# Performance work log

Measured on AMD Instinct MI355X. Metric: run time of the kernel, lower is better.

## Reference

```python
import jax, jax.numpy as jnp
import numpy as np

N_NODES = 1_000_000
N_EDGES = 32_000_000
NUM_HOP = 3


def setup_inputs() -> dict:
    key = jax.random.key(0)
    k1, k2 = jax.random.split(key)
    h = jnp.ones((N_NODES, 1), dtype=jnp.float32)  # graph.ndata['one']
    src = jax.random.randint(k1, (N_EDGES,), 0, N_NODES, dtype=jnp.int64 if jax.config.read('jax_enable_x64') else jnp.int32)
    dst = jax.random.randint(k2, (N_EDGES,), 0, N_NODES, dtype=jnp.int64 if jax.config.read('jax_enable_x64') else jnp.int32)
    # SAGEConv weights, init to ones per reset_parameters(); bias=False
    w_self = jnp.ones((NUM_HOP, 1, 1), dtype=jnp.float32)
    w_neigh = jnp.ones((NUM_HOP, 1, 1), dtype=jnp.float32)
    return {"h": h, "src": src, "dst": dst, "w_self": w_self, "w_neigh": w_neigh}


def reference(h, src, dst, w_self, w_neigh):
    # Stacked SAGEConv(aggregator='add', bias=False, feat_drop=0):
    #   h_out = h @ W_self + segment_sum(h[src] -> dst) @ W_neigh
    # dropout p=0 between layers is identity.
    n = h.shape[0]
    num_hop = w_self.shape[0]
    for i in range(num_hop):
        neigh = jax.ops.segment_sum(h[src], dst, num_segments=n)  # [N, F] sum over in-edges
        h = h @ w_self[i] + neigh @ w_neigh[i]
    return h
```

## Files before the change

kernel.cpp:

```cpp
#include <hip/hip_runtime.h>


typedef unsigned u32x4 __attribute__((ext_vector_type(4)));
typedef float    f32x4 __attribute__((ext_vector_type(4)));

constexpr int BLK      = 256;
constexpr int BBITS    = 13;
constexpr int BUCKET   = 1 << BBITS;
constexpr int SEGSHIFT = 17;
constexpr int NSEG     = 8;
constexpr int SEGB     = 3;
constexpr int KMAX     = 1024;
constexpr int SPLIT    = 4;
constexpr int TILE     = 8192;
constexpr int HBLOCKS  = 1024;
constexpr unsigned SRCMASK = (1u << SEGSHIFT) - 1u;


__global__ void zero_u32(unsigned* __restrict__ p, int n) {
    int i = blockIdx.x * blockDim.x + threadIdx.x;
    if (i < n) p[i] = 0u;
}

__global__ void hist_kernel(const int* __restrict__ dst, const int* __restrict__ src,
                            int ne, unsigned* __restrict__ count, int nk) {
    __shared__ unsigned hist[KMAX * 4];
    for (int b = threadIdx.x; b < KMAX * 4; b += blockDim.x) hist[b] = 0u;
    __syncthreads();
    const u32x4* dst4 = reinterpret_cast<const u32x4*>(dst);
    const u32x4* src4 = reinterpret_cast<const u32x4*>(src);
    int nvec = ne >> 2;
    int sub = threadIdx.x & 3;
    for (int i = blockIdx.x * blockDim.x + threadIdx.x; i < nvec;
         i += gridDim.x * blockDim.x) {
        u32x4 d = __builtin_nontemporal_load(dst4 + i);
        u32x4 s = __builtin_nontemporal_load(src4 + i);
        atomicAdd(&hist[((((d.x >> BBITS) << SEGB) | (s.x >> SEGSHIFT)) << 2) | sub], 1u);
        atomicAdd(&hist[((((d.y >> BBITS) << SEGB) | (s.y >> SEGSHIFT)) << 2) | sub], 1u);
        atomicAdd(&hist[((((d.z >> BBITS) << SEGB) | (s.z >> SEGSHIFT)) << 2) | sub], 1u);
        atomicAdd(&hist[((((d.w >> BBITS) << SEGB) | (s.w >> SEGSHIFT)) << 2) | sub], 1u);
    }
    if (blockIdx.x == 0 && threadIdx.x == 0)
        for (int i = nvec << 2; i < ne; ++i) {
            unsigned key = (((unsigned)dst[i] >> BBITS) << SEGB) |
                           ((unsigned)src[i] >> SEGSHIFT);
            atomicAdd(&hist[key << 2], 1u);
        }
    __syncthreads();
    for (int b = threadIdx.x; b < nk; b += blockDim.x) {
        unsigned v = hist[b * 4] + hist[b * 4 + 1] + hist[b * 4 + 2] + hist[b * 4 + 3];
        if (v) atomicAdd(&count[b], v);
    }
}

__global__ void scan_kernel(const unsigned* __restrict__ count,
                            unsigned* __restrict__ offsets,
                            unsigned* __restrict__ cursor, int nk) {
    __shared__ unsigned s[KMAX];
    int t = threadIdx.x;
    unsigned v  = (t < nk) ? count[t] : 0u;
    unsigned pv = (v + 3u) & ~3u;
    s[t] = pv;
    __syncthreads();
    for (int d = 1; d < KMAX; d <<= 1) {
        unsigned u = (t >= d) ? s[t - d] : 0u;
        __syncthreads();
        s[t] += u;
        __syncthreads();
    }
    unsigned excl = s[t] - pv;
    if (t < nk) { offsets[t] = excl; cursor[t] = excl; }
}

__global__ __launch_bounds__(1024)
void bin_kernel(const int* __restrict__ src, const int* __restrict__ dst, int ne,
                unsigned* __restrict__ cursor, unsigned* __restrict__ recs) {
    __shared__ unsigned hist[KMAX];
    __shared__ unsigned start[KMAX];
    __shared__ unsigned lpos[KMAX];
    __shared__ unsigned rec[TILE];
    __shared__ unsigned short kid[TILE];

    int base = blockIdx.x * TILE;
    int cnt = min(TILE, ne - base);
    if (cnt <= 0) return;

    hist[threadIdx.x] = 0u;
    __syncthreads();

    int nvec = cnt & ~3;
    const u32x4* dst4 = reinterpret_cast<const u32x4*>(dst + base);
    const u32x4* src4 = reinterpret_cast<const u32x4*>(src + base);

    for (int i = threadIdx.x; i < (nvec >> 2); i += blockDim.x) {
        u32x4 d = dst4[i];
        u32x4 s = src4[i];
        atomicAdd(&hist[((d.x >> BBITS) << SEGB) | (s.x >> SEGSHIFT)], 1u);
        atomicAdd(&hist[((d.y >> BBITS) << SEGB) | (s.y >> SEGSHIFT)], 1u);
        atomicAdd(&hist[((d.z >> BBITS) << SEGB) | (s.z >> SEGSHIFT)], 1u);
        atomicAdd(&hist[((d.w >> BBITS) << SEGB) | (s.w >> SEGSHIFT)], 1u);
    }
    if (threadIdx.x == 0)
        for (int i = nvec; i < cnt; ++i) {
            unsigned key = (((unsigned)dst[base + i] >> BBITS) << SEGB) |
                           ((unsigned)src[base + i] >> SEGSHIFT);
            atomicAdd(&hist[key], 1u);
        }
    __syncthreads();

    {
        int t = threadIdx.x;
        unsigned v = hist[t];
        start[t] = v;
        __syncthreads();
        for (int d = 1; d < KMAX; d <<= 1) {
            unsigned u = (t >= d) ? start[t - d] : 0u;
            __syncthreads();
            start[t] += u;
            __syncthreads();
        }
        unsigned excl = start[t] - v;
        __syncthreads();
        start[t] = excl;
        lpos[t]  = excl;
        if (v) hist[t] = atomicAdd(&cursor[t], v);
        __syncthreads();
    }

    for (int i = threadIdx.x; i < (nvec >> 2); i += blockDim.x) {
        u32x4 d = __builtin_nontemporal_load(dst4 + i);
        u32x4 s = __builtin_nontemporal_load(src4 + i);
        unsigned dd[4] = {d.x, d.y, d.z, d.w};
        unsigned ss[4] = {s.x, s.y, s.z, s.w};
#pragma unroll
        for (int k = 0; k < 4; ++k) {
            unsigned key = ((dd[k] >> BBITS) << SEGB) | (ss[k] >> SEGSHIFT);
            unsigned p = atomicAdd(&lpos[key], 1u);
            rec[p] = ((dd[k] & (BUCKET - 1)) << SEGSHIFT) | (ss[k] & SRCMASK);
            kid[p] = (unsigned short)key;
        }
    }
    if (threadIdx.x == 0)
        for (int i = nvec; i < cnt; ++i) {
            unsigned dd = (unsigned)dst[base + i], ss = (unsigned)src[base + i];
            unsigned key = ((dd >> BBITS) << SEGB) | (ss >> SEGSHIFT);
            unsigned p = atomicAdd(&lpos[key], 1u);
            rec[p] = ((dd & (BUCKET - 1)) << SEGSHIFT) | (ss & SRCMASK);
            kid[p] = (unsigned short)key;
        }
    __syncthreads();

    for (int i = threadIdx.x; i < cnt; i += blockDim.x) {
        int k = kid[i];
        recs[hist[k] + ((unsigned)i - start[k])] = rec[i];
    }
}

__global__ __launch_bounds__(1024, 8)
void agg_kernel(const float* __restrict__ curh,
                const unsigned* __restrict__ recs,
                const unsigned* __restrict__ offsets,
                const unsigned* __restrict__ count,
                float* __restrict__ partials) {
    __shared__ float acc[BUCKET];
    int b = blockIdx.x >> 2;
    int s = blockIdx.x & 3;
    for (int i = threadIdx.x; i < BUCKET; i += 1024) acc[i] = 0.0f;
    __syncthreads();
#pragma unroll 1
    for (int seg = 0; seg < NSEG; ++seg) {
        unsigned k   = ((unsigned)b << SEGB) | (unsigned)seg;
        unsigned bs  = offsets[k];
        unsigned cnt = count[k];
        unsigned qlen = (cnt >> 2) & ~3u;
        unsigned ss = bs + (unsigned)s * qlen;
        unsigned sc = (s == SPLIT - 1) ? (cnt - 3u * qlen) : qlen;
        const float* ch = curh + ((unsigned)seg << SEGSHIFT);
        unsigned n4 = sc >> 2;
        const u32x4* rq = reinterpret_cast<const u32x4*>(recs + ss);
        for (unsigned q = threadIdx.x; q < n4; q += 1024) {
            u32x4 r = __builtin_nontemporal_load(rq + q);
            float v0 = ch[r.x & SRCMASK];
            float v1 = ch[r.y & SRCMASK];
            float v2 = ch[r.z & SRCMASK];
            float v3 = ch[r.w & SRCMASK];
            atomicAdd(&acc[r.x >> SEGSHIFT], v0);
            atomicAdd(&acc[r.y >> SEGSHIFT], v1);
            atomicAdd(&acc[r.z >> SEGSHIFT], v2);
            atomicAdd(&acc[r.w >> SEGSHIFT], v3);
        }
        if (s == SPLIT - 1) {
            unsigned tb = ss + (n4 << 2);
            unsigned rem = sc & 3u;
            if (threadIdx.x < rem) {
                unsigned r = recs[tb + threadIdx.x];
                atomicAdd(&acc[r >> SEGSHIFT], ch[r & SRCMASK]);
            }
        }
    }
    __syncthreads();
    float* outp = partials + ((size_t)blockIdx.x) * BUCKET;
    for (int i = threadIdx.x; i < BUCKET; i += 1024)
        __builtin_nontemporal_store(acc[i], outp + i);
}

__global__ void reduce_combine(const float* __restrict__ curh,
                               const float* __restrict__ partials,
                               const float* __restrict__ w_self,
                               const float* __restrict__ w_neigh, int hop,
                               float* __restrict__ out, int n) {
    int i = blockIdx.x * blockDim.x + threadIdx.x;
    int nq = (n + 3) >> 2;
    if (i >= nq) return;
    int node = i << 2;
    float wsv = w_self[hop], wnv = w_neigh[hop];
    int b = node >> BBITS, l = node & (BUCKET - 1);
    const float* p0 = partials + ((size_t)b * SPLIT) * BUCKET + l;
    if (node + 3 < n) {
        f32x4 a0 = __builtin_nontemporal_load(reinterpret_cast<const f32x4*>(p0));
        f32x4 a1 = __builtin_nontemporal_load(reinterpret_cast<const f32x4*>(p0 + BUCKET));
        f32x4 a2 = __builtin_nontemporal_load(reinterpret_cast<const f32x4*>(p0 + 2 * BUCKET));
        f32x4 a3 = __builtin_nontemporal_load(reinterpret_cast<const f32x4*>(p0 + 3 * BUCKET));
        f32x4 hh = *reinterpret_cast<const f32x4*>(curh + node);
        f32x4 o = hh * wsv + ((a0 + a1) + (a2 + a3)) * wnv;
        *reinterpret_cast<f32x4*>(out + node) = o;
    } else {
        for (int j = node; j < n; ++j) {
            int bb = j >> BBITS, ll = j & (BUCKET - 1);
            const float* pp = partials + ((size_t)bb * SPLIT) * BUCKET + ll;
            out[j] = curh[j] * wsv +
                     (pp[0] + pp[BUCKET] + pp[2 * BUCKET] + pp[3 * BUCKET]) * wnv;
        }
    }
}


__global__ void zero_f32(float* __restrict__ p, int n) {
    int i = blockIdx.x * blockDim.x + threadIdx.x;
    if (i < n) p[i] = 0.0f;
}

__global__ void scatter_add(const float* __restrict__ h, const int* __restrict__ src,
                            const int* __restrict__ dst, float* __restrict__ neigh, int ne) {
    int i = blockIdx.x * blockDim.x + threadIdx.x;
    int base = i * 4;
    if (base + 3 < ne) {
        int4 s = *reinterpret_cast<const int4*>(src + base);
        int4 d = *reinterpret_cast<const int4*>(dst + base);
        atomicAdd(&neigh[d.x], h[s.x]);
        atomicAdd(&neigh[d.y], h[s.y]);
        atomicAdd(&neigh[d.z], h[s.z]);
        atomicAdd(&neigh[d.w], h[s.w]);
    } else if (base < ne) {
        for (int e = base; e < ne; ++e) atomicAdd(&neigh[dst[e]], h[src[e]]);
    }
}

__global__ void combine(const float* __restrict__ h, const float* __restrict__ neigh,
                        const float* __restrict__ w_self, const float* __restrict__ w_neigh,
                        int hop, float* __restrict__ out, int n) {
    int i = blockIdx.x * blockDim.x + threadIdx.x;
    if (i < n) out[i] = h[i] * w_self[hop] + neigh[i] * w_neigh[hop];
}


extern "C" void kernel_launch(void* const* d_in, const int* in_sizes, int n_in,
                              void* d_out, int out_size, void* d_ws, size_t ws_size,
                              hipStream_t stream) {
    const float* h       = (const float*)d_in[0];
    const int*   src     = (const int*)d_in[1];
    const int*   dst     = (const int*)d_in[2];
    const float* w_self  = (const float*)d_in[3];
    const float* w_neigh = (const float*)d_in[4];
    float* out = (float*)d_out;

    const int n    = in_sizes[0];
    const int ne   = in_sizes[1];
    const int hops = in_sizes[3];

    const int nb = (n + BUCKET - 1) >> BBITS;
    const int nk = nb * NSEG;

    size_t off = 0;
    auto take = [&](size_t bytes) { size_t o = off; off = (off + bytes + 255) & ~255UL; return o; };
    size_t o_recs     = take(((size_t)ne + 4 * KMAX) * 4);
    size_t o_count    = take((size_t)KMAX * 4);
    size_t o_offsets  = take((size_t)KMAX * 4);
    size_t o_cursor   = take((size_t)KMAX * 4);
    size_t o_partials = take((size_t)nb * SPLIT * BUCKET * 4);
    size_t o_buf      = take((size_t)n * 4);
    size_t needed = off;

    char* ws = (char*)d_ws;
    bool fast = (ws_size >= needed) && (nk <= KMAX) && (n <= (1 << 20));

    if (fast) {
        unsigned* recs     = (unsigned*)(ws + o_recs);
        unsigned* count    = (unsigned*)(ws + o_count);
        unsigned* offsets  = (unsigned*)(ws + o_offsets);
        unsigned* cursor   = (unsigned*)(ws + o_cursor);
        float*    partials = (float*)(ws + o_partials);
        float*    buf      = (float*)(ws + o_buf);

        zero_u32<<<(KMAX + BLK - 1) / BLK, BLK, 0, stream>>>(count, KMAX);
        hist_kernel<<<HBLOCKS, BLK, 0, stream>>>(dst, src, ne, count, nk);
        scan_kernel<<<1, KMAX, 0, stream>>>(count, offsets, cursor, nk);
        bin_kernel<<<(ne + TILE - 1) / TILE, KMAX, 0, stream>>>(src, dst, ne, cursor, recs);

        const int nq = (n + 3) >> 2;
        const int gridQ = (nq + BLK - 1) / BLK;
        const float* cur = h;
        for (int hop = 0; hop < hops; ++hop) {
            float* nxt = (hop == hops - 1) ? out : buf;
            agg_kernel<<<nb * SPLIT, 1024, 0, stream>>>(cur, recs, offsets, count, partials);
            reduce_combine<<<gridQ, BLK, 0, stream>>>(cur, partials, w_self, w_neigh, hop, nxt, n);
            cur = nxt;
        }
    } else {
        float* buf   = (float*)d_ws;
        float* neigh = buf + n;
        const int gridN = (n + BLK - 1) / BLK;
        const int gridE = ((ne + 3) / 4 + BLK - 1) / BLK;
        const float* cur = h;
        for (int hop = 0; hop < hops; ++hop) {
            float* nxt = (hop == hops - 1) ? out : buf;
            zero_f32<<<gridN, BLK, 0, stream>>>(neigh, n);
            scatter_add<<<gridE, BLK, 0, stream>>>(cur, src, dst, neigh, ne);
            combine<<<gridN, BLK, 0, stream>>>(cur, neigh, w_self, w_neigh, hop, nxt, n);
            cur = nxt;
        }
    }
}
```

Before: 941.3 us.

## Bin edges by destination bucket only and software-pipeline the aggregation gathers

Drops the source-segment dimension from the binning key, so records are grouped only by 4096-node destination buckets. The source index is packed into 20 bits alongside the local destination. The histogram pass no longer reads src, the binning kernel moves to 256-thread blocks, and aggregation uses a 2-way split with a double-buffered loop that issues the next gathers before applying the LDS atomics. This cuts index traffic and per-segment loop overhead. In exchange, gathers into h now span the whole 4MB array instead of a 512KB source segment, which risks worse cache locality.

```diff
diff --git a/kernel.cpp b/kernel.cpp
--- a/kernel.cpp
+++ b/kernel.cpp
@@ -4,17 +4,13 @@
 typedef unsigned u32x4 __attribute__((ext_vector_type(4)));
 typedef float    f32x4 __attribute__((ext_vector_type(4)));
 
-constexpr int BLK      = 256;
-constexpr int BBITS    = 13;
-constexpr int BUCKET   = 1 << BBITS;
-constexpr int SEGSHIFT = 17;
-constexpr int NSEG     = 8;
-constexpr int SEGB     = 3;
-constexpr int KMAX     = 1024;
-constexpr int SPLIT    = 4;
-constexpr int TILE     = 8192;
-constexpr int HBLOCKS  = 1024;
-constexpr unsigned SRCMASK = (1u << SEGSHIFT) - 1u;
+constexpr int BLK     = 256;
+constexpr int BBITS   = 12;
+constexpr int BUCKET  = 1 << BBITS;
+constexpr int NB_MAX  = 256;
+constexpr int SPLIT   = 2;
+constexpr int TILE    = 8192;
+constexpr int HBLOCKS = 1024;
 
 
 __global__ void zero_u32(unsigned* __restrict__ p, int n) {
@@ -22,32 +18,27 @@
     if (i < n) p[i] = 0u;
 }
 
-__global__ void hist_kernel(const int* __restrict__ dst, const int* __restrict__ src,
-                            int ne, unsigned* __restrict__ count, int nk) {
-    __shared__ unsigned hist[KMAX * 4];
-    for (int b = threadIdx.x; b < KMAX * 4; b += blockDim.x) hist[b] = 0u;
+__global__ void hist_kernel(const int* __restrict__ dst, int ne,
+                            unsigned* __restrict__ count, int nb) {
+    __shared__ unsigned hist[NB_MAX * 4];
+    for (int b = threadIdx.x; b < NB_MAX * 4; b += blockDim.x) hist[b] = 0u;
     __syncthreads();
     const u32x4* dst4 = reinterpret_cast<const u32x4*>(dst);
-    const u32x4* src4 = reinterpret_cast<const u32x4*>(src);
     int nvec = ne >> 2;
     int sub = threadIdx.x & 3;
     for (int i = blockIdx.x * blockDim.x + threadIdx.x; i < nvec;
          i += gridDim.x * blockDim.x) {
         u32x4 d = __builtin_nontemporal_load(dst4 + i);
-        u32x4 s = __builtin_nontemporal_load(src4 + i);
-        atomicAdd(&hist[((((d.x >> BBITS) << SEGB) | (s.x >> SEGSHIFT)) << 2) | sub], 1u);
-        atomicAdd(&hist[((((d.y >> BBITS) << SEGB) | (s.y >> SEGSHIFT)) << 2) | sub], 1u);
-        atomicAdd(&hist[((((d.z >> BBITS) << SEGB) | (s.z >> SEGSHIFT)) << 2) | sub], 1u);
-        atomicAdd(&hist[((((d.w >> BBITS) << SEGB) | (s.w >> SEGSHIFT)) << 2) | sub], 1u);
+        atomicAdd(&hist[((d.x >> BBITS) << 2) | sub], 1u);
+        atomicAdd(&hist[((d.y >> BBITS) << 2) | sub], 1u);
+        atomicAdd(&hist[((d.z >> BBITS) << 2) | sub], 1u);
+        atomicAdd(&hist[((d.w >> BBITS) << 2) | sub], 1u);
     }
     if (blockIdx.x == 0 && threadIdx.x == 0)
-        for (int i = nvec << 2; i < ne; ++i) {
-            unsigned key = (((unsigned)dst[i] >> BBITS) << SEGB) |
-                           ((unsigned)src[i] >> SEGSHIFT);
-            atomicAdd(&hist[key << 2], 1u);
-        }
-    __syncthreads();
-    for (int b = threadIdx.x; b < nk; b += blockDim.x) {
+        for (int i = nvec << 2; i < ne; ++i)
+            atomicAdd(&hist[(((unsigned)dst[i] >> BBITS) << 2)], 1u);
+    __syncthreads();
+    for (int b = threadIdx.x; b < nb; b += blockDim.x) {
         unsigned v = hist[b * 4] + hist[b * 4 + 1] + hist[b * 4 + 2] + hist[b * 4 + 3];
         if (v) atomicAdd(&count[b], v);
     }
@@ -55,37 +46,38 @@
 
 __global__ void scan_kernel(const unsigned* __restrict__ count,
                             unsigned* __restrict__ offsets,
-                            unsigned* __restrict__ cursor, int nk) {
-    __shared__ unsigned s[KMAX];
+                            unsigned* __restrict__ cursor, int nb) {
+    __shared__ unsigned s[NB_MAX];
     int t = threadIdx.x;
-    unsigned v  = (t < nk) ? count[t] : 0u;
+    unsigned v  = (t < nb) ? count[t] : 0u;
     unsigned pv = (v + 3u) & ~3u;
     s[t] = pv;
     __syncthreads();
-    for (int d = 1; d < KMAX; d <<= 1) {
+    for (int d = 1; d < NB_MAX; d <<= 1) {
         unsigned u = (t >= d) ? s[t - d] : 0u;
         __syncthreads();
         s[t] += u;
         __syncthreads();
     }
     unsigned excl = s[t] - pv;
-    if (t < nk) { offsets[t] = excl; cursor[t] = excl; }
-}
-
-__global__ __launch_bounds__(1024)
+    if (t < nb) { offsets[t] = excl; cursor[t] = excl; }
+}
+
+__global__ __launch_bounds__(256)
 void bin_kernel(const int* __restrict__ src, const int* __restrict__ dst, int ne,
                 unsigned* __restrict__ cursor, unsigned* __restrict__ recs) {
-    __shared__ unsigned hist[KMAX];
-    __shared__ unsigned start[KMAX];
-    __shared__ unsigned lpos[KMAX];
+    __shared__ unsigned hist[NB_MAX];
+    __shared__ unsigned start[NB_MAX];
+    __shared__ unsigned lpos[NB_MAX];
+    __shared__ unsigned gbase[NB_MAX];
     __shared__ unsigned rec[TILE];
-    __shared__ unsigned short kid[TILE];
+    __shared__ unsigned char bid[TILE];
 
     int base = blockIdx.x * TILE;
     int cnt = min(TILE, ne - base);
     if (cnt <= 0) return;
 
-    hist[threadIdx.x] = 0u;
+    for (int b = threadIdx.x; b < NB_MAX; b += blockDim.x) hist[b] = 0u;
     __syncthreads();
 
     int nvec = cnt & ~3;
@@ -94,18 +86,14 @@
 
     for (int i = threadIdx.x; i < (nvec >> 2); i += blockDim.x) {
         u32x4 d = dst4[i];
-        u32x4 s = src4[i];
-        atomicAdd(&hist[((d.x >> BBITS) << SEGB) | (s.x >> SEGSHIFT)], 1u);
-        atomicAdd(&hist[((d.y >> BBITS) << SEGB) | (s.y >> SEGSHIFT)], 1u);
-        atomicAdd(&hist[((d.z >> BBITS) << SEGB) | (s.z >> SEGSHIFT)], 1u);
-        atomicAdd(&hist[((d.w >> BBITS) << SEGB) | (s.w >> SEGSHIFT)], 1u);
+        atomicAdd(&hist[d.x >> BBITS], 1u);
+        atomicAdd(&hist[d.y >> BBITS], 1u);
+        atomicAdd(&hist[d.z >> BBITS], 1u);
+        atomicAdd(&hist[d.w >> BBITS], 1u);
     }
     if (threadIdx.x == 0)
-        for (int i = nvec; i < cnt; ++i) {
-            unsigned key = (((unsigned)dst[base + i] >> BBITS) << SEGB) |
-                           ((unsigned)src[base + i] >> SEGSHIFT);
-            atomicAdd(&hist[key], 1u);
-        }
+        for (int i = nvec; i < cnt; ++i)
+            atomicAdd(&hist[(unsigned)dst[base + i] >> BBITS], 1u);
     __syncthreads();
 
     {
@@ -113,7 +101,7 @@
         unsigned v = hist[t];
         start[t] = v;
         __syncthreads();
-        for (int d = 1; d < KMAX; d <<= 1) {
+        for (int d = 1; d < NB_MAX; d <<= 1) {
             unsigned u = (t >= d) ? start[t - d] : 0u;
             __syncthreads();
             start[t] += u;
@@ -123,7 +111,7 @@
         __syncthreads();
         start[t] = excl;
         lpos[t]  = excl;
-        if (v) hist[t] = atomicAdd(&cursor[t], v);
+        if (v) gbase[t] = atomicAdd(&cursor[t], v);
         __syncthreads();
     }
 
@@ -134,25 +122,25 @@
         unsigned ss[4] = {s.x, s.y, s.z, s.w};
 #pragma unroll
         for (int k = 0; k < 4; ++k) {
-            unsigned key = ((dd[k] >> BBITS) << SEGB) | (ss[k] >> SEGSHIFT);
-            unsigned p = atomicAdd(&lpos[key], 1u);
-            rec[p] = ((dd[k] & (BUCKET - 1)) << SEGSHIFT) | (ss[k] & SRCMASK);
-            kid[p] = (unsigned short)key;
+            unsigned b = dd[k] >> BBITS;
+            unsigned p = atomicAdd(&lpos[b], 1u);
+            rec[p] = ((dd[k] & (BUCKET - 1)) << 20) | ss[k];
+            bid[p] = (unsigned char)b;
         }
     }
     if (threadIdx.x == 0)
         for (int i = nvec; i < cnt; ++i) {
             unsigned dd = (unsigned)dst[base + i], ss = (unsigned)src[base + i];
-            unsigned key = ((dd >> BBITS) << SEGB) | (ss >> SEGSHIFT);
-            unsigned p = atomicAdd(&lpos[key], 1u);
-            rec[p] = ((dd & (BUCKET - 1)) << SEGSHIFT) | (ss & SRCMASK);
-            kid[p] = (unsigned short)key;
+            unsigned b = dd >> BBITS;
+            unsigned p = atomicAdd(&lpos[b], 1u);
+            rec[p] = ((dd & (BUCKET - 1)) << 20) | ss;
+            bid[p] = (unsigned char)b;
         }
     __syncthreads();
 
     for (int i = threadIdx.x; i < cnt; i += blockDim.x) {
-        int k = kid[i];
-        recs[hist[k] + ((unsigned)i - start[k])] = rec[i];
+        int b = bid[i];
+        recs[gbase[b] + ((unsigned)i - start[b])] = rec[i];
     }
 }
 
@@ -163,40 +151,77 @@
                 const unsigned* __restrict__ count,
                 float* __restrict__ partials) {
     __shared__ float acc[BUCKET];
-    int b = blockIdx.x >> 2;
-    int s = blockIdx.x & 3;
+    int b = blockIdx.x >> 1;
+    int s = blockIdx.x & 1;
     for (int i = threadIdx.x; i < BUCKET; i += 1024) acc[i] = 0.0f;
     __syncthreads();
-#pragma unroll 1
-    for (int seg = 0; seg < NSEG; ++seg) {
-        unsigned k   = ((unsigned)b << SEGB) | (unsigned)seg;
-        unsigned bs  = offsets[k];
-        unsigned cnt = count[k];
-        unsigned qlen = (cnt >> 2) & ~3u;
-        unsigned ss = bs + (unsigned)s * qlen;
-        unsigned sc = (s == SPLIT - 1) ? (cnt - 3u * qlen) : qlen;
-        const float* ch = curh + ((unsigned)seg << SEGSHIFT);
-        unsigned n4 = sc >> 2;
-        const u32x4* rq = reinterpret_cast<const u32x4*>(recs + ss);
-        for (unsigned q = threadIdx.x; q < n4; q += 1024) {
-            u32x4 r = __builtin_nontemporal_load(rq + q);
-            float v0 = ch[r.x & SRCMASK];
-            float v1 = ch[r.y & SRCMASK];
-            float v2 = ch[r.z & SRCMASK];
-            float v3 = ch[r.w & SRCMASK];
-            atomicAdd(&acc[r.x >> SEGSHIFT], v0);
-            atomicAdd(&acc[r.y >> SEGSHIFT], v1);
-            atomicAdd(&acc[r.z >> SEGSHIFT], v2);
-            atomicAdd(&acc[r.w >> SEGSHIFT], v3);
-        }
-        if (s == SPLIT - 1) {
-            unsigned tb = ss + (n4 << 2);
-            unsigned rem = sc & 3u;
-            if (threadIdx.x < rem) {
-                unsigned r = recs[tb + threadIdx.x];
-                atomicAdd(&acc[r >> SEGSHIFT], ch[r & SRCMASK]);
-            }
-        }
+    unsigned bs  = offsets[b];
+    unsigned cnt = count[b];
+    unsigned half = (cnt >> 1) & ~3u;
+    unsigned ss = bs + (s ? half : 0u);
+    unsigned sc = s ? (cnt - half) : half;
+    unsigned n4 = sc >> 2;
+    const u32x4* rq = reinterpret_cast<const u32x4*>(recs + ss);
+
+    unsigned q = threadIdx.x;
+    if (q + 1024 < n4) {
+        u32x4 rA = __builtin_nontemporal_load(rq + q);
+        u32x4 rB = __builtin_nontemporal_load(rq + q + 1024);
+        float a0 = curh[rA.x & 0xFFFFFu];
+        float a1 = curh[rA.y & 0xFFFFFu];
+        float a2 = curh[rA.z & 0xFFFFFu];
+        float a3 = curh[rA.w & 0xFFFFFu];
+        float b0 = curh[rB.x & 0xFFFFFu];
+        float b1 = curh[rB.y & 0xFFFFFu];
+        float b2 = curh[rB.z & 0xFFFFFu];
+        float b3 = curh[rB.w & 0xFFFFFu];
+        q += 2048;
+        for (; q + 1024 < n4; q += 2048) {
+            u32x4 rA2 = __builtin_nontemporal_load(rq + q);
+            u32x4 rB2 = __builtin_nontemporal_load(rq + q + 1024);
+            atomicAdd(&acc[rA.x >> 20], a0);
+            atomicAdd(&acc[rA.y >> 20], a1);
+            atomicAdd(&acc[rA.z >> 20], a2);
+            atomicAdd(&acc[rA.w >> 20], a3);
+            atomicAdd(&acc[rB.x >> 20], b0);
+            atomicAdd(&acc[rB.y >> 20], b1);
+            atomicAdd(&acc[rB.z >> 20], b2);
+            atomicAdd(&acc[rB.w >> 20], b3);
+            rA = rA2; rB = rB2;
+            a0 = curh[rA.x & 0xFFFFFu];
+            a1 = curh[rA.y & 0xFFFFFu];
+            a2 = curh[rA.z & 0xFFFFFu];
+            a3 = curh[rA.w & 0xFFFFFu];
+            b0 = curh[rB.x & 0xFFFFFu];
+            b1 = curh[rB.y & 0xFFFFFu];
+            b2 = curh[rB.z & 0xFFFFFu];
+            b3 = curh[rB.w & 0xFFFFFu];
+        }
+        atomicAdd(&acc[rA.x >> 20], a0);
+        atomicAdd(&acc[rA.y >> 20], a1);
+        atomicAdd(&acc[rA.z >> 20], a2);
+        atomicAdd(&acc[rA.w >> 20], a3);
+        atomicAdd(&acc[rB.x >> 20], b0);
+        atomicAdd(&acc[rB.y >> 20], b1);
+        atomicAdd(&acc[rB.z >> 20], b2);
+        atomicAdd(&acc[rB.w >> 20], b3);
+    }
+    if (q < n4) {
+        u32x4 r = __builtin_nontemporal_load(rq + q);
+        float v0 = curh[r.x & 0xFFFFFu];
+        float v1 = curh[r.y & 0xFFFFFu];
+        float v2 = curh[r.z & 0xFFFFFu];
+        float v3 = curh[r.w & 0xFFFFFu];
+        atomicAdd(&acc[r.x >> 20], v0);
+        atomicAdd(&acc[r.y >> 20], v1);
+        atomicAdd(&acc[r.z >> 20], v2);
+        atomicAdd(&acc[r.w >> 20], v3);
+    }
+    unsigned tb = ss + (n4 << 2);
+    unsigned rem = sc & 3u;
+    if (threadIdx.x < rem) {
+        unsigned r = recs[tb + threadIdx.x];
+        atomicAdd(&acc[r >> 20], curh[r & 0xFFFFFu]);
     }
     __syncthreads();
     float* outp = partials + ((size_t)blockIdx.x) * BUCKET;
@@ -216,20 +241,18 @@
     float wsv = w_self[hop], wnv = w_neigh[hop];
     int b = node >> BBITS, l = node & (BUCKET - 1);
     const float* p0 = partials + ((size_t)b * SPLIT) * BUCKET + l;
+    const float* p1 = p0 + BUCKET;
     if (node + 3 < n) {
-        f32x4 a0 = __builtin_nontemporal_load(reinterpret_cast<const f32x4*>(p0));
-        f32x4 a1 = __builtin_nontemporal_load(reinterpret_cast<const f32x4*>(p0 + BUCKET));
-        f32x4 a2 = __builtin_nontemporal_load(reinterpret_cast<const f32x4*>(p0 + 2 * BUCKET));
-        f32x4 a3 = __builtin_nontemporal_load(reinterpret_cast<const f32x4*>(p0 + 3 * BUCKET));
+        f32x4 a = __builtin_nontemporal_load(reinterpret_cast<const f32x4*>(p0));
+        f32x4 c = __builtin_nontemporal_load(reinterpret_cast<const f32x4*>(p1));
         f32x4 hh = *reinterpret_cast<const f32x4*>(curh + node);
-        f32x4 o = hh * wsv + ((a0 + a1) + (a2 + a3)) * wnv;
+        f32x4 o = hh * wsv + (a + c) * wnv;
         *reinterpret_cast<f32x4*>(out + node) = o;
     } else {
         for (int j = node; j < n; ++j) {
             int bb = j >> BBITS, ll = j & (BUCKET - 1);
             const float* pp = partials + ((size_t)bb * SPLIT) * BUCKET + ll;
-            out[j] = curh[j] * wsv +
-                     (pp[0] + pp[BUCKET] + pp[2 * BUCKET] + pp[3 * BUCKET]) * wnv;
+            out[j] = curh[j] * wsv + (pp[0] + pp[BUCKET]) * wnv;
         }
     }
 }
@@ -279,20 +302,19 @@
     const int hops = in_sizes[3];
 
     const int nb = (n + BUCKET - 1) >> BBITS;
-    const int nk = nb * NSEG;
 
     size_t off = 0;
     auto take = [&](size_t bytes) { size_t o = off; off = (off + bytes + 255) & ~255UL; return o; };
-    size_t o_recs     = take(((size_t)ne + 4 * KMAX) * 4);
-    size_t o_count    = take((size_t)KMAX * 4);
-    size_t o_offsets  = take((size_t)KMAX * 4);
-    size_t o_cursor   = take((size_t)KMAX * 4);
+    size_t o_recs     = take(((size_t)ne + 4 * NB_MAX) * 4);
+    size_t o_count    = take((size_t)NB_MAX * 4);
+    size_t o_offsets  = take((size_t)NB_MAX * 4);
+    size_t o_cursor   = take((size_t)NB_MAX * 4);
     size_t o_partials = take((size_t)nb * SPLIT * BUCKET * 4);
     size_t o_buf      = take((size_t)n * 4);
     size_t needed = off;
 
     char* ws = (char*)d_ws;
-    bool fast = (ws_size >= needed) && (nk <= KMAX) && (n <= (1 << 20));
+    bool fast = (ws_size >= needed) && (nb <= NB_MAX) && (n <= (1 << 20));
 
     if (fast) {
         unsigned* recs     = (unsigned*)(ws + o_recs);
@@ -302,10 +324,10 @@
         float*    partials = (float*)(ws + o_partials);
         float*    buf      = (float*)(ws + o_buf);
 
-        zero_u32<<<(KMAX + BLK - 1) / BLK, BLK, 0, stream>>>(count, KMAX);
-        hist_kernel<<<HBLOCKS, BLK, 0, stream>>>(dst, src, ne, count, nk);
-        scan_kernel<<<1, KMAX, 0, stream>>>(count, offsets, cursor, nk);
-        bin_kernel<<<(ne + TILE - 1) / TILE, KMAX, 0, stream>>>(src, dst, ne, cursor, recs);
+        zero_u32<<<1, NB_MAX, 0, stream>>>(count, NB_MAX);
+        hist_kernel<<<HBLOCKS, BLK, 0, stream>>>(dst, ne, count, nb);
+        scan_kernel<<<1, NB_MAX, 0, stream>>>(count, offsets, cursor, nb);
+        bin_kernel<<<(ne + TILE - 1) / TILE, BLK, 0, stream>>>(src, dst, ne, cursor, recs);
 
         const int nq = (n + 3) >> 2;
         const int gridQ = (nq + BLK - 1) / BLK;
```

Result: no change. 924.2 us (-1.8%).
